# Kernel tuning notes

Measured on AMD Instinct MI355X. Metric: run time of the kernel, lower is better.

Reference implementation:

```python
import jax, jax.numpy as jnp
import numpy as np

N, IN_XC, IN_YC, OUTC, H, W = 8, 512, 256, 256, 96, 96
C2 = OUTC // 2  # 128
K = 3
NUM_LAT = K * K // 2 + 1  # 5


def conv2d(x, w, b=None, pad=0):
    out = jax.lax.conv_general_dilated(
        x, w, window_strides=(1, 1), padding=[(pad, pad), (pad, pad)],
        dimension_numbers=('NCHW', 'OIHW', 'NCHW'))
    if b is not None:
        out = out + b[None, :, None, None]
    return out


def patches3x3(x):
    # torch nn.Unfold(3, padding=1) taps, ordered (kh, kw) row-major -> [N,C,9,H,W]
    n, c, h, w = x.shape
    xp = jnp.pad(x, ((0, 0), (0, 0), (1, 1), (1, 1)))
    cols = [xp[:, :, i:i + h, j:j + w] for i in range(3) for j in range(3)]
    return jnp.stack(cols, axis=2)


def pool_to_3x3(x):
    # AdaptiveAvgPool2d(3) with H,W divisible by 3 == mean over equal bins
    n, c, h, w = x.shape
    return x.reshape(n, c, 3, h // 3, 3, w // 3).mean(axis=(3, 5))


def setup_inputs() -> dict:
    key = jax.random.key(0)
    ks = jax.random.split(key, 24)
    g = lambda i, shape, s=0.05: (jax.random.normal(ks[i], shape, dtype=jnp.float32) * s)
    return {
        'x': jax.random.normal(ks[0], (N, IN_XC, H, W), dtype=jnp.float32),
        'y': jax.random.normal(ks[1], (N, IN_YC, H, W), dtype=jnp.float32),
        # SDFM.down_input: 1x1 conv in_xC -> out_C
        'w_down': g(2, (OUTC, IN_XC, 1, 1)), 'b_down': g(3, (OUTC,)),
        # channel-attention MLP over 3x3 pooled grid
        'w_ce': g(4, (NUM_LAT, K * K)), 'w_gd': g(5, (K * K, NUM_LAT)),
        'bn_g': jnp.ones((C2,), jnp.float32), 'bn_b': jnp.zeros((C2,), jnp.float32),
        # gernerate_kernel_channel: 1x1 conv mid_in_yC -> mid_in_xC (both 128)
        'w_kc': g(6, (C2, C2, 1, 1)), 'b_kc': g(7, (C2,)),
        # gernerate_kernel_spatial: 3x3 conv C2->C2 then 1x1 conv C2->9
        'w_ks1': g(8, (C2, C2, 3, 3)), 'b_ks1': g(9, (C2,)),
        'w_ks2': g(10, (K * K, C2, 1, 1)), 'b_ks2': g(11, (K * K,)),
        # spatial-attention convs (bias=False)
        'w_sp1': g(12, (1, C2, 3, 3)), 'w_sp': g(13, (1, 2, 3, 3)),
        # branch fuse: 3x3 conv out_C -> out_C
        'w_fb': g(14, (OUTC, 2 * C2, 3, 3)), 'b_fb': g(15, (OUTC,)),
        # SDFM.fuse (BasicConv_PRelu): 3x3 conv 2*out_C -> out_C, BN(eval), PReLU
        'w_fuse': g(16, (OUTC, 2 * OUTC, 3, 3)),
        'bn2_g': jnp.ones((OUTC,), jnp.float32), 'bn2_b': jnp.zeros((OUTC,), jnp.float32),
        'prelu_a': jnp.full((OUTC,), 0.25, jnp.float32),
    }


def reference(x, y, w_down, b_down, w_ce, w_gd, bn_g, bn_b, w_kc, b_kc,
              w_ks1, b_ks1, w_ks2, b_ks2, w_sp1, w_sp, w_fb, b_fb,
              w_fuse, bn2_g, bn2_b, prelu_a):
    # SDFM.down_input
    x = conv2d(x, w_down, b_down, pad=0)          # [N, 256, H, W]
    n, c, h, w = x.shape
    c2 = c // 2
    x1, x2 = x[:, :c2], x[:, c2:]                 # [N,128,H,W] each
    y1, y2 = y[:, :c2], y[:, c2:]

    # --- channel branch: per-(sample,channel) dynamic 3x3 depthwise kernel ---
    gl = pool_to_3x3(x1).reshape(n, c2, K * K)    # [N,128,9]
    att = gl @ w_ce.T                              # ce (no bias) -> [N,128,5]
    att = att * bn_g[None, :, None] + bn_b[None, :, None]  # BN1d eval (rm=0, rv=1)
    att = jax.nn.relu(att)
    att = jax.nn.sigmoid(att @ w_gd.T)            # [N,128,9]

    kc = conv2d(pool_to_3x3(y1), w_kc, b_kc, pad=0)  # [N,128,3,3]
    kc = kc.reshape(n, c2, K * K) * att           # [N,128,9]
    # grouped conv (groups = N*C/2) == per-sample depthwise dynamic conv
    channel_after = jnp.einsum('nckhw,nck->nchw', patches3x3(x1), kc)

    # --- spatial branch: per-pixel dynamic 3x3 kernel ---
    ks = conv2d(conv2d(y2, w_ks1, b_ks1, pad=1), w_ks2, b_ks2, pad=0)  # [N,9,H,W]

    ksp = conv2d(x2, w_sp1, None, pad=1)          # [N,1,H,W]
    p = patches3x3(ksp).reshape(n, K * K, h, w)   # [N,9,H,W]
    avg = p.mean(axis=1, keepdims=True)
    mx = p.max(axis=1, keepdims=True)
    sp = jax.nn.sigmoid(conv2d(jnp.concatenate([avg, mx], axis=1), w_sp, None, pad=1))  # [N,1,H,W]

    kernel_after = (ks * sp).transpose(0, 2, 3, 1)[..., None]  # [N,H,W,9,1]

    # faithful replication of the original quirky reshape of unfold output:
    # [N, C2*9, H*W] -> [N, H, W, C2, 9]
    unfold_x = patches3x3(x2).reshape(n, c2 * K * K, h * w).reshape(n, h, w, c2, K * K)
    spatial_after = jnp.matmul(unfold_x, kernel_after)[..., 0]  # [N,H,W,C2]
    spatial_after = spatial_after.transpose(0, 3, 1, 2)          # [N,C2,H,W]

    result = jnp.concatenate([channel_after, spatial_after], axis=1)  # [N,256,H,W]
    r1 = conv2d(result, w_fb, b_fb, pad=1)        # branch fuse 3x3

    # SDFM.fuse: BasicConv_PRelu = conv3x3 (no bias) + BN(eval, rm=0,rv=1) + PReLU
    o = conv2d(jnp.concatenate([x, r1], axis=1), w_fuse, None, pad=1)
    o = o * bn2_g[None, :, None, None] + bn2_b[None, :, None, None]
    o = jnp.where(o >= 0, o, prelu_a[None, :, None, None] * o)
    return o
```

## Files before the change

### kernel.cpp

```cpp
#include <hip/hip_runtime.h>
#include <hip/hip_bf16.h>
#include <math.h>

#define HW 9216
#define IMG 96

typedef __bf16 bf16x8 __attribute__((ext_vector_type(8)));
typedef float  f32x4  __attribute__((ext_vector_type(4)));

__device__ __forceinline__ void gload16(const void* g, void* l) {
    __builtin_amdgcn_global_load_lds((const unsigned int*)g, (unsigned int*)l, 16, 0, 0);
}

#define WAITV(N) asm volatile("s_waitcnt vmcnt(" #N ")" ::: "memory")
#define BARX()   { asm volatile("" ::: "memory"); __builtin_amdgcn_s_barrier(); asm volatile("" ::: "memory"); }

__global__ __launch_bounds__(256) void nchw2nhwc_kernel(
    const float* __restrict__ src, long n_stride_src,
    __hip_bfloat16* __restrict__ dst, int dst_stride)
{
    __shared__ float tile[32][65];
    const int px0 = blockIdx.x * 64;
    const int c0  = blockIdx.y * 32;
    const int n   = blockIdx.z;
    const int tid = threadIdx.x;
    const int tx = tid & 63, ty = tid >> 6;
    #pragma unroll
    for (int i = 0; i < 8; ++i)
        tile[ty + i * 4][tx] = src[n * n_stride_src + (long)(c0 + ty + i * 4) * HW + px0 + tx];
    __syncthreads();
    const int ci = tid & 31, pxl = tid >> 5;
    #pragma unroll
    for (int j = 0; j < 8; ++j) {
        int px = pxl + j * 8;
        dst[((long)n * HW + px0 + px) * dst_stride + c0 + ci] = __float2bfloat16(tile[ci][px]);
    }
}

__global__ __launch_bounds__(256) void wconv_kernel(
    const float* __restrict__ src, __hip_bfloat16* __restrict__ dst,
    int cout, int cin, int taps)
{
    int idx = blockIdx.x * 256 + threadIdx.x;
    if (idx >= cout * cin) return;
    int co = idx / cin, ci = idx % cin;
    for (int t = 0; t < taps; ++t)
        dst[((long)t * cout + co) * cin + ci] = __float2bfloat16(src[(long)idx * taps + t]);
}

template<int CIN, int TAPS, bool SPLIT>
__global__ __launch_bounds__(256, 2) void mfma_conv(
    const __hip_bfloat16* __restrict__ in_a,
    const __hip_bfloat16* __restrict__ in_b,
    const __hip_bfloat16* __restrict__ w_t,
    const float* __restrict__ bias,
    float* __restrict__ out_nchw, long nchw_nstride,
    __hip_bfloat16* __restrict__ out_nhwc, int nhwc_stride,
    int cout,
    const float* __restrict__ bng, const float* __restrict__ bnb,
    const float* __restrict__ pra,
    const __hip_bfloat16* __restrict__ zeropage)
{
    constexpr int ROWS = (TAPS == 9) ? 6 : 4;
    constexpr int COLS = (TAPS == 9) ? 98 : 96;
    constexpr int HOFF = (TAPS == 9) ? 1 : 0;
    constexpr int PSTR = SPLIT ? 256 : CIN;
    constexpr int NSEG_IN = ROWS * COLS * 4;
    constexpr int NSEG_W  = TAPS * 64 * 4;
    constexpr int IN_BYTES = NSEG_IN * 16;
    constexpr int W_BYTES  = NSEG_W * 16;
    constexpr int BUF = IN_BYTES + W_BYTES;
    constexpr int NCHUNK = CIN / 32;
    constexpr int FULL_IN = NSEG_IN / 256;
    constexpr int HAS_TAIL = (NSEG_IN % 256) != 0;
    constexpr int IT_IN = FULL_IN + HAS_TAIL;
    constexpr int IT_W  = NSEG_W / 256;

    extern __shared__ __align__(16) char lds[];

    const int h0   = blockIdx.x * 4;
    const int cob  = blockIdx.y * 64;
    const int n    = blockIdx.z;
    const int tid  = threadIdx.x;
    const int lane = tid & 63;
    const int wave = tid >> 6;
    const int l16  = lane & 15, lg = lane >> 4;

    const long dAB = SPLIT ? ((const char*)in_b - (const char*)in_a - 448) : 0;

    const char* inptr[IT_IN];
    int inval[IT_IN];
    #pragma unroll
    for (int t = 0; t < IT_IN; ++t) {
        int seg = tid + t * 256;
        int s2 = (seg < NSEG_IN) ? seg : 0;
        int pix = s2 >> 2, qp = s2 & 3;
        int r = pix / COLS, c = pix % COLS;
        int h = h0 + r - HOFF, w = c - HOFF;
        int q = qp ^ ((c >> 1) & 3);
        bool valid = (h >= 0 && h < IMG && w >= 0 && w < IMG);
        inptr[t] = valid
            ? (const char*)(in_a + ((long)n * HW + h * IMG + w) * PSTR + q * 8)
            : (const char*)zeropage;
        inval[t] = valid ? 1 : 0;
    }
    const char* wptr[IT_W];
    #pragma unroll
    for (int t = 0; t < IT_W; ++t) {
        int seg = tid + t * 256;
        int tap = seg >> 8, rem = seg & 255;
        int co = rem >> 2, qp = rem & 3;
        int q = qp ^ ((co >> 1) & 3);
        wptr[t] = (const char*)(w_t + ((long)tap * cout + cob + co) * CIN + q * 8);
    }

    auto stage = [&](int bb, long adv) {
        char* ib = lds + bb * BUF;
        char* wb = ib + IN_BYTES;
        #pragma unroll
        for (int t = 0; t < FULL_IN; ++t) {
            int seg = tid + t * 256;
            gload16(inptr[t], ib + seg * 16);
            if (inval[t]) inptr[t] += adv;
        }
        if (HAS_TAIL) {
            int seg = tid + FULL_IN * 256;
            if (seg < NSEG_IN) {
                gload16(inptr[IT_IN - 1], ib + seg * 16);
                if (inval[IT_IN - 1]) inptr[IT_IN - 1] += adv;
            }
        }
        #pragma unroll
        for (int t = 0; t < IT_W; ++t) {
            int seg = tid + t * 256;
            gload16(wptr[t], wb + seg * 16);
            wptr[t] += 64;
        }
    };

    f32x4 acc[4][6];
    #pragma unroll
    for (int m = 0; m < 4; ++m)
        #pragma unroll
        for (int nf = 0; nf < 6; ++nf) acc[m][nf] = (f32x4){0.f, 0.f, 0.f, 0.f};

    const int qa = lg ^ ((l16 >> 1) & 3);
    const int a_off = l16 * 64 + qa * 16;

    stage(0, 64);

    for (int ch = 0; ch < NCHUNK; ++ch) {
        if (ch + 1 < NCHUNK) {
            long adv = (SPLIT && (ch + 1) == 7) ? dAB : 64;
            stage((ch + 1) & 1, adv);
            if constexpr (TAPS == 9) {
                if (wave == 0) { WAITV(19); } else { WAITV(18); }
            } else {
                WAITV(7);
            }
        } else {
            WAITV(0);
        }
        BARX();

        const char* ib = lds + (ch & 1) * BUF;
        const char* wb = ib + IN_BYTES;
        __builtin_amdgcn_s_setprio(1);
        #pragma unroll
        for (int tap = 0; tap < TAPS; ++tap) {
            const int g = (TAPS == 9) ? tap / 3 : 0;
            const int kx = (TAPS == 9) ? tap % 3 : 0;
            bf16x8 a[4];
            #pragma unroll
            for (int m = 0; m < 4; ++m)
                a[m] = *(const bf16x8*)(wb + tap * 4096 + m * 1024 + a_off);
            #pragma unroll
            for (int nf = 0; nf < 6; ++nf) {
                const int c = nf * 16 + l16 + kx;
                const int qb = lg ^ ((c >> 1) & 3);
                bf16x8 b = *(const bf16x8*)(ib + ((wave + g) * COLS + c) * 64 + qb * 16);
                #pragma unroll
                for (int m = 0; m < 4; ++m)
                    acc[m][nf] = __builtin_amdgcn_mfma_f32_16x16x32_bf16(a[m], b, acc[m][nf], 0, 0, 0);
            }
        }
        __builtin_amdgcn_s_setprio(0);
        BARX();
    }

    const int hrow = h0 + wave;
    #pragma unroll
    for (int m = 0; m < 4; ++m) {
        const int co = cob + m * 16 + lg * 4;
        float bs[4], g4[4], b4[4], p4[4];
        #pragma unroll
        for (int r = 0; r < 4; ++r) bs[r] = bias ? bias[co + r] : 0.f;
        if (bng) {
            #pragma unroll
            for (int r = 0; r < 4; ++r) { g4[r] = bng[co + r]; b4[r] = bnb[co + r]; p4[r] = pra[co + r]; }
        }
        #pragma unroll
        for (int nf = 0; nf < 6; ++nf) {
            const int wcol = nf * 16 + l16;
            const long px = (long)hrow * IMG + wcol;
            float v[4];
            #pragma unroll
            for (int r = 0; r < 4; ++r) {
                v[r] = acc[m][nf][r] + bs[r];
                if (bng) {
                    v[r] = v[r] * g4[r] + b4[r];
                    v[r] = (v[r] >= 0.f) ? v[r] : p4[r] * v[r];
                }
            }
            if (out_nchw) {
                #pragma unroll
                for (int r = 0; r < 4; ++r)
                    out_nchw[(long)n * nchw_nstride + (long)(co + r) * HW + px] = v[r];
            }
            if (out_nhwc) {
                union { __hip_bfloat16 h[4]; uint2 u; } pk;
                #pragma unroll
                for (int r = 0; r < 4; ++r) pk.h[r] = __float2bfloat16(v[r]);
                *reinterpret_cast<uint2*>(&out_nhwc[((long)n * HW + px) * nhwc_stride + co]) = pk.u;
            }
        }
    }
}

__global__ __launch_bounds__(256) void pool_kernel(
    const float* __restrict__ xd, const float* __restrict__ y,
    float* __restrict__ gl, float* __restrict__ py)
{
    const int c = blockIdx.x, n = blockIdx.y, which = blockIdx.z;
    const int tid = threadIdx.x;
    const float* src = (which == 0) ? (xd + ((long)n * 256 + c) * HW)
                                    : (y  + ((long)n * 256 + c) * HW);
    float local[9];
    #pragma unroll
    for (int k = 0; k < 9; ++k) local[k] = 0.f;
    for (int i = tid; i < HW; i += 256) {
        int h = i / 96, w = i % 96;
        local[(h / 32) * 3 + (w / 32)] += src[i];
    }
    __shared__ float red[9][4];
    const int wv = tid >> 6, lane = tid & 63;
    #pragma unroll
    for (int k = 0; k < 9; ++k) {
        float v = local[k];
        for (int off = 32; off > 0; off >>= 1) v += __shfl_down(v, off, 64);
        if (lane == 0) red[k][wv] = v;
    }
    __syncthreads();
    if (tid < 9) {
        float s = (red[tid][0] + red[tid][1] + red[tid][2] + red[tid][3]) * (1.f / 1024.f);
        float* dst = (which == 0) ? gl : py;
        dst[((long)n * 128 + c) * 9 + tid] = s;
    }
}

__global__ __launch_bounds__(128) void attkc_kernel(
    const float* __restrict__ gl, const float* __restrict__ py,
    const float* __restrict__ w_ce, const float* __restrict__ w_gd,
    const float* __restrict__ bng, const float* __restrict__ bnb,
    const float* __restrict__ w_kc, const float* __restrict__ b_kc,
    float* __restrict__ kc)
{
    const int n = blockIdx.x, c = threadIdx.x;
    __shared__ float py_s[128][9];
    #pragma unroll
    for (int k = 0; k < 9; ++k) py_s[c][k] = py[((long)n * 128 + c) * 9 + k];
    __syncthreads();
    float g[9];
    #pragma unroll
    for (int k = 0; k < 9; ++k) g[k] = gl[((long)n * 128 + c) * 9 + k];
    float t[5];
    #pragma unroll
    for (int l = 0; l < 5; ++l) {
        float s = 0.f;
        #pragma unroll
        for (int k = 0; k < 9; ++k) s += g[k] * w_ce[l * 9 + k];
        s = s * bng[c] + bnb[c];
        t[l] = s > 0.f ? s : 0.f;
    }
    float att[9];
    #pragma unroll
    for (int k = 0; k < 9; ++k) {
        float s = 0.f;
        #pragma unroll
        for (int l = 0; l < 5; ++l) s += t[l] * w_gd[k * 5 + l];
        att[k] = 1.f / (1.f + expf(-s));
    }
    float kc0[9];
    float bk = b_kc[c];
    #pragma unroll
    for (int k = 0; k < 9; ++k) kc0[k] = bk;
    for (int c2 = 0; c2 < 128; ++c2) {
        float wv = w_kc[c * 128 + c2];
        #pragma unroll
        for (int k = 0; k < 9; ++k) kc0[k] += wv * py_s[c2][k];
    }
    #pragma unroll
    for (int k = 0; k < 9; ++k)
        kc[((long)n * 128 + c) * 9 + k] = kc0[k] * att[k];
}

__global__ __launch_bounds__(256) void channel_nhwc_kernel(
    const __hip_bfloat16* __restrict__ catx, const float* __restrict__ kc,
    __hip_bfloat16* __restrict__ catfb)
{
    const int h  = blockIdx.x;
    const int n  = blockIdx.y;
    const int cg = (threadIdx.x & 15) * 8;
    const int w0 = threadIdx.x >> 4;
    float k9[8][9];
    #pragma unroll
    for (int j = 0; j < 8; ++j)
        #pragma unroll
        for (int t = 0; t < 9; ++t) k9[j][t] = kc[((long)n * 128 + cg + j) * 9 + t];
    const long pbase = (long)n * HW;
    for (int it = 0; it < 6; ++it) {
        const int w = w0 + it * 16;
        float acc[8];
        #pragma unroll
        for (int j = 0; j < 8; ++j) acc[j] = 0.f;
        #pragma unroll
        for (int ky = 0; ky < 3; ++ky) {
            const int hh = h + ky - 1;
            if (hh < 0 || hh >= IMG) continue;
            #pragma unroll
            for (int kx = 0; kx < 3; ++kx) {
                const int ww = w + kx - 1;
                if (ww < 0 || ww >= IMG) continue;
                bf16x8 v = *reinterpret_cast<const bf16x8*>(
                    &catx[(pbase + hh * IMG + ww) * 256 + cg]);
                #pragma unroll
                for (int j = 0; j < 8; ++j)
                    acc[j] += k9[j][ky * 3 + kx] * (float)v[j];
            }
        }
        union { __hip_bfloat16 hh[8]; uint4 u; } pk;
        #pragma unroll
        for (int j = 0; j < 8; ++j) pk.hh[j] = __float2bfloat16(acc[j]);
        *reinterpret_cast<uint4*>(&catfb[(pbase + h * IMG + w) * 256 + cg]) = pk.u;
    }
}

__global__ __launch_bounds__(256) void ks_kernel(
    const float* __restrict__ ksmid, const float* __restrict__ w_ks2,
    const float* __restrict__ b_ks2, float* __restrict__ ks)
{
    __shared__ float w_s[9 * 128];
    const int tid = threadIdx.x;
    for (int i = tid; i < 1152; i += 256) w_s[i] = w_ks2[i];
    __syncthreads();
    const int p = blockIdx.x * 256 + tid;
    const int n = blockIdx.y;
    float acc[9];
    #pragma unroll
    for (int k = 0; k < 9; ++k) acc[k] = b_ks2[k];
    for (int c = 0; c < 128; ++c) {
        float v = ksmid[((long)n * 128 + c) * HW + p];
        #pragma unroll
        for (int k = 0; k < 9; ++k) acc[k] += w_s[k * 128 + c] * v;
    }
    #pragma unroll
    for (int k = 0; k < 9; ++k) ks[((long)n * 9 + k) * HW + p] = acc[k];
}

__global__ __launch_bounds__(256) void ksp_nhwc_kernel(
    const __hip_bfloat16* __restrict__ catx, const float* __restrict__ w_sp1,
    float* __restrict__ ksp)
{
    __shared__ float w_s[9][128];
    const int tid = threadIdx.x;
    for (int i = tid; i < 1152; i += 256) {
        int ci = i / 9, tap = i % 9;
        w_s[tap][ci] = w_sp1[i];
    }
    __syncthreads();
    const int p = blockIdx.x * 256 + tid;
    const int n = blockIdx.y;
    const int h = p / 96, w = p % 96;
    const long pbase = (long)n * HW;
    float acc = 0.f;
    #pragma unroll
    for (int ky = 0; ky < 3; ++ky) {
        const int hh = h + ky - 1;
        if (hh < 0 || hh >= IMG) continue;
        #pragma unroll
        for (int kx = 0; kx < 3; ++kx) {
            const int ww = w + kx - 1;
            if (ww < 0 || ww >= IMG) continue;
            const int tap = ky * 3 + kx;
            const __hip_bfloat16* row = &catx[(pbase + hh * IMG + ww) * 256 + 128];
            #pragma unroll
            for (int vq = 0; vq < 16; ++vq) {
                bf16x8 v = *reinterpret_cast<const bf16x8*>(&row[vq * 8]);
                #pragma unroll
                for (int j = 0; j < 8; ++j)
                    acc += w_s[tap][vq * 8 + j] * (float)v[j];
            }
        }
    }
    ksp[pbase + p] = acc;
}

__global__ __launch_bounds__(256) void sp_kernel(
    const float* __restrict__ ksp, const float* __restrict__ w_sp,
    float* __restrict__ sp)
{
    const int p = blockIdx.x * 256 + threadIdx.x;
    const int n = blockIdx.y;
    const int h = p / 96, w = p % 96;
    const float* kp = ksp + (long)n * HW;
    float acc = 0.f;
    #pragma unroll
    for (int dy = 0; dy < 3; ++dy)
        #pragma unroll
        for (int dx = 0; dx < 3; ++dx) {
            int hh = h + dy - 1, ww = w + dx - 1;
            if (hh < 0 || hh >= 96 || ww < 0 || ww >= 96) continue;
            float s = 0.f, m = -1e30f;
            #pragma unroll
            for (int iy = 0; iy < 3; ++iy)
                #pragma unroll
                for (int ix = 0; ix < 3; ++ix) {
                    int h2 = hh + iy - 1, w2 = ww + ix - 1;
                    float v = (h2 >= 0 && h2 < 96 && w2 >= 0 && w2 < 96) ? kp[h2 * 96 + w2] : 0.f;
                    s += v; m = fmaxf(m, v);
                }
            acc += w_sp[dy * 3 + dx] * (s * (1.f / 9.f)) + w_sp[9 + dy * 3 + dx] * m;
        }
    sp[(long)n * HW + p] = 1.f / (1.f + expf(-acc));
}

__global__ __launch_bounds__(256) void spatial_kernel(
    const float* __restrict__ xd, const float* __restrict__ ks,
    const float* __restrict__ sp, __hip_bfloat16* __restrict__ catfb)
{
    const int cc = blockIdx.x;
    const int n  = blockIdx.y;
    const int tid = threadIdx.x;
    __shared__ float plane[HW];
    const float* src = xd + ((long)n * 256 + 128 + cc) * HW;
    for (int i = tid; i < HW / 4; i += 256)
        *reinterpret_cast<float4*>(&plane[i * 4]) = *reinterpret_cast<const float4*>(&src[i * 4]);
    __syncthreads();
    const int c  = tid & 127;
    const int pr = tid >> 7;
    const int c9 = c * 9;
    for (int j = 0; j < 36; ++j) {
        const int pl = pr + j * 2;
        const int p  = cc * 72 + pl;
        float spv = sp[(long)n * HW + p];
        float kv[9];
        #pragma unroll
        for (int k = 0; k < 9; ++k) kv[k] = ks[((long)n * 9 + k) * HW + p] * spv;
        const int base = pl * 1152 + c9;
        int kk0 = base / 9216;
        int r20 = base - kk0 * 9216;
        int h20 = r20 / 96;
        int w20 = r20 - h20 * 96;
        float acc = 0.f;
        #pragma unroll
        for (int k = 0; k < 9; ++k) {
            int kk = kk0, h2 = h20, w2 = w20 + k;
            if (w2 >= 96) { h2 += 1; w2 -= 96; }
            if (h2 >= 96) { kk += 1; h2 -= 96; }
            int hh = h2 + kk / 3 - 1;
            int ww = w2 + kk % 3 - 1;
            float v = (hh >= 0 && hh < 96 && ww >= 0 && ww < 96) ? plane[hh * 96 + ww] : 0.f;
            acc += v * kv[k];
        }
        catfb[((long)n * HW + p) * 256 + 128 + c] = __float2bfloat16(acc);
    }
}

extern "C" void kernel_launch(void* const* d_in, const int* in_sizes, int n_in,
                              void* d_out, int out_size, void* d_ws, size_t ws_size,
                              hipStream_t stream)
{
    const float* x      = (const float*)d_in[0];
    const float* y      = (const float*)d_in[1];
    const float* w_down = (const float*)d_in[2];
    const float* b_down = (const float*)d_in[3];
    const float* w_ce   = (const float*)d_in[4];
    const float* w_gd   = (const float*)d_in[5];
    const float* bn_g   = (const float*)d_in[6];
    const float* bn_b   = (const float*)d_in[7];
    const float* w_kc   = (const float*)d_in[8];
    const float* b_kc   = (const float*)d_in[9];
    const float* w_ks1  = (const float*)d_in[10];
    const float* b_ks1  = (const float*)d_in[11];
    const float* w_ks2  = (const float*)d_in[12];
    const float* b_ks2  = (const float*)d_in[13];
    const float* w_sp1  = (const float*)d_in[14];
    const float* w_sp   = (const float*)d_in[15];
    const float* w_fb   = (const float*)d_in[16];
    const float* b_fb   = (const float*)d_in[17];
    const float* w_fuse = (const float*)d_in[18];
    const float* bn2_g  = (const float*)d_in[19];
    const float* bn2_b  = (const float*)d_in[20];
    const float* prelu  = (const float*)d_in[21];
    float* out = (float*)d_out;
    char* ws = (char*)d_ws;

    const long HWl = HW;
    float* xd = (float*)ws;                               ws += 8L * 256 * HWl * 4;
    char* region2 = ws;                                   ws += 8L * HWl * 512 * 2;
    __hip_bfloat16* x_t    = (__hip_bfloat16*)region2;
    __hip_bfloat16* cat_r1 = (__hip_bfloat16*)region2;
    float*          ksmid  = (float*)region2;
    __hip_bfloat16* catfb  = (__hip_bfloat16*)(region2 + 8L * HWl * 256 * 2);
    __hip_bfloat16* cat_x  = (__hip_bfloat16*)ws;         ws += 8L * HWl * 256 * 2;
    __hip_bfloat16* y2t    = (__hip_bfloat16*)ws;         ws += 8L * HWl * 128 * 2;
    __hip_bfloat16* wdown_bf = (__hip_bfloat16*)ws;       ws += 1L * 256 * 512 * 2;
    __hip_bfloat16* wks1_bf  = (__hip_bfloat16*)ws;       ws += 9L * 128 * 128 * 2;
    __hip_bfloat16* wfb_bf   = (__hip_bfloat16*)ws;       ws += 9L * 256 * 256 * 2;
    __hip_bfloat16* wfuse_bf = (__hip_bfloat16*)ws;       ws += 9L * 256 * 512 * 2;
    float* ks   = (float*)ws;  ws += 8L * 9 * HWl * 4;
    float* ksp  = (float*)ws;  ws += 8L * HWl * 4;
    float* spb  = (float*)ws;  ws += 8L * HWl * 4;
    float* gl   = (float*)ws;  ws += 8L * 128 * 9 * 4;
    float* py   = (float*)ws;  ws += 8L * 128 * 9 * 4;
    float* kc   = (float*)ws;  ws += 8L * 128 * 9 * 4;
    __hip_bfloat16* zp = (__hip_bfloat16*)ws;  ws += 256;

    hipMemsetAsync((void*)zp, 0, 256, stream);

    wconv_kernel<<<dim3(512), 256, 0, stream>>>(w_down, wdown_bf, 256, 512, 1);
    wconv_kernel<<<dim3(64),  256, 0, stream>>>(w_ks1,  wks1_bf,  128, 128, 9);
    wconv_kernel<<<dim3(256), 256, 0, stream>>>(w_fb,   wfb_bf,   256, 256, 9);
    wconv_kernel<<<dim3(512), 256, 0, stream>>>(w_fuse, wfuse_bf, 256, 512, 9);

    nchw2nhwc_kernel<<<dim3(144, 16, 8), 256, 0, stream>>>(x, 512L * HWl, x_t, 512);
    mfma_conv<512, 1, false><<<dim3(24, 4, 8), 256, 57344, stream>>>(
        x_t, nullptr, wdown_bf, b_down, xd, 256L * HWl, cat_x, 256, 256,
        nullptr, nullptr, nullptr, zp);

    nchw2nhwc_kernel<<<dim3(144, 4, 8), 256, 0, stream>>>(y + 128L * HWl, 256L * HWl, y2t, 128);

    pool_kernel<<<dim3(128, 8, 2), 256, 0, stream>>>(xd, y, gl, py);
    attkc_kernel<<<dim3(8), 128, 0, stream>>>(gl, py, w_ce, w_gd, bn_g, bn_b, w_kc, b_kc, kc);

    mfma_conv<128, 9, false><<<dim3(24, 2, 8), 256, 148992, stream>>>(
        y2t, nullptr, wks1_bf, b_ks1, ksmid, 128L * HWl, nullptr, 0, 128,
        nullptr, nullptr, nullptr, zp);
    ks_kernel<<<dim3(36, 8), 256, 0, stream>>>(ksmid, w_ks2, b_ks2, ks);

    ksp_nhwc_kernel<<<dim3(36, 8), 256, 0, stream>>>(cat_x, w_sp1, ksp);
    sp_kernel<<<dim3(36, 8), 256, 0, stream>>>(ksp, w_sp, spb);

    spatial_kernel<<<dim3(128, 8), 256, 0, stream>>>(xd, ks, spb, catfb);
    channel_nhwc_kernel<<<dim3(96, 8), 256, 0, stream>>>(cat_x, kc, catfb);

    mfma_conv<256, 9, false><<<dim3(24, 4, 8), 256, 148992, stream>>>(
        catfb, nullptr, wfb_bf, b_fb, nullptr, 0, cat_r1, 256, 256,
        nullptr, nullptr, nullptr, zp);

    mfma_conv<512, 9, true><<<dim3(24, 4, 8), 256, 148992, stream>>>(
        cat_x, cat_r1, wfuse_bf, nullptr, out, 256L * HWl, nullptr, 0, 256,
        bn2_g, bn2_b, prelu, zp);
}
```

Baseline: 678.1 us.

## Load conv weights directly into registers and software-pipeline by tap group

```diff
diff --git a/kernel.cpp b/kernel.cpp
--- a/kernel.cpp
+++ b/kernel.cpp
@@ -12,8 +12,9 @@
     __builtin_amdgcn_global_load_lds((const unsigned int*)g, (unsigned int*)l, 16, 0, 0);
 }
 
-#define WAITV(N) asm volatile("s_waitcnt vmcnt(" #N ")" ::: "memory")
+#define WAITV0() asm volatile("s_waitcnt vmcnt(0)" ::: "memory")
 #define BARX()   { asm volatile("" ::: "memory"); __builtin_amdgcn_s_barrier(); asm volatile("" ::: "memory"); }
+#define SB0()    __builtin_amdgcn_sched_barrier(0)
 
 __global__ __launch_bounds__(256) void nchw2nhwc_kernel(
     const float* __restrict__ src, long n_stride_src,
@@ -66,15 +67,13 @@
     constexpr int HOFF = (TAPS == 9) ? 1 : 0;
     constexpr int PSTR = SPLIT ? 256 : CIN;
     constexpr int NSEG_IN = ROWS * COLS * 4;
-    constexpr int NSEG_W  = TAPS * 64 * 4;
     constexpr int IN_BYTES = NSEG_IN * 16;
-    constexpr int W_BYTES  = NSEG_W * 16;
-    constexpr int BUF = IN_BYTES + W_BYTES;
     constexpr int NCHUNK = CIN / 32;
     constexpr int FULL_IN = NSEG_IN / 256;
     constexpr int HAS_TAIL = (NSEG_IN % 256) != 0;
     constexpr int IT_IN = FULL_IN + HAS_TAIL;
-    constexpr int IT_W  = NSEG_W / 256;
+    constexpr int TPG = (TAPS == 9) ? 3 : 1;
+    constexpr int NW = TPG * 4;
 
     extern __shared__ __align__(16) char lds[];
 
@@ -104,19 +103,9 @@
             : (const char*)zeropage;
         inval[t] = valid ? 1 : 0;
     }
-    const char* wptr[IT_W];
-    #pragma unroll
-    for (int t = 0; t < IT_W; ++t) {
-        int seg = tid + t * 256;
-        int tap = seg >> 8, rem = seg & 255;
-        int co = rem >> 2, qp = rem & 3;
-        int q = qp ^ ((co >> 1) & 3);
-        wptr[t] = (const char*)(w_t + ((long)tap * cout + cob + co) * CIN + q * 8);
-    }
 
     auto stage = [&](int bb, long adv) {
-        char* ib = lds + bb * BUF;
-        char* wb = ib + IN_BYTES;
+        char* ib = lds + bb * IN_BYTES;
         #pragma unroll
         for (int t = 0; t < FULL_IN; ++t) {
             int seg = tid + t * 256;
@@ -130,63 +119,85 @@
                 if (inval[IT_IN - 1]) inptr[IT_IN - 1] += adv;
             }
         }
-        #pragma unroll
-        for (int t = 0; t < IT_W; ++t) {
-            int seg = tid + t * 256;
-            gload16(wptr[t], wb + seg * 16);
-            wptr[t] += 64;
-        }
     };
 
+    const __hip_bfloat16* wlane = w_t + (long)(cob + l16) * CIN + lg * 8;
+
     f32x4 acc[4][6];
     #pragma unroll
     for (int m = 0; m < 4; ++m)
         #pragma unroll
         for (int nf = 0; nf < 6; ++nf) acc[m][nf] = (f32x4){0.f, 0.f, 0.f, 0.f};
 
-    const int qa = lg ^ ((l16 >> 1) & 3);
-    const int a_off = l16 * 64 + qa * 16;
+    bf16x8 wA[NW], wB[NW];
+
+#define LOADW(WREG, CI0, G)                                                   \
+    _Pragma("unroll")                                                         \
+    for (int t3 = 0; t3 < TPG; ++t3)                                          \
+        _Pragma("unroll")                                                     \
+        for (int m = 0; m < 4; ++m)                                           \
+            WREG[t3 * 4 + m] = *(const bf16x8*)(wlane +                       \
+                ((long)(((G) * TPG + t3) * cout + m * 16)) * CIN + (CI0));
+
+#define MFMAG(WREG, IB, G)                                                    \
+    __builtin_amdgcn_s_setprio(1);                                            \
+    _Pragma("unroll")                                                         \
+    for (int t3 = 0; t3 < TPG; ++t3) {                                        \
+        _Pragma("unroll")                                                     \
+        for (int nf = 0; nf < 6; ++nf) {                                      \
+            const int c = nf * 16 + l16 + ((TAPS == 9) ? t3 : 0);             \
+            const int qb = lg ^ ((c >> 1) & 3);                               \
+            bf16x8 b = *(const bf16x8*)((IB) +                                \
+                (((wave + (G)) * COLS) + c) * 64 + qb * 16);                  \
+            _Pragma("unroll")                                                 \
+            for (int m = 0; m < 4; ++m)                                       \
+                acc[m][nf] = __builtin_amdgcn_mfma_f32_16x16x32_bf16(         \
+                    WREG[t3 * 4 + m], b, acc[m][nf], 0, 0, 0);                \
+        }                                                                     \
+    }                                                                         \
+    __builtin_amdgcn_s_setprio(0);
 
     stage(0, 64);
-
-    for (int ch = 0; ch < NCHUNK; ++ch) {
-        if (ch + 1 < NCHUNK) {
-            long adv = (SPLIT && (ch + 1) == 7) ? dAB : 64;
-            stage((ch + 1) & 1, adv);
-            if constexpr (TAPS == 9) {
-                if (wave == 0) { WAITV(19); } else { WAITV(18); }
-            } else {
-                WAITV(7);
-            }
+    LOADW(wA, 0, 0);
+    WAITV0(); BARX();
+
+    const char* ib0 = lds;
+    const char* ib1 = lds + IN_BYTES;
+
+    for (int pc = 0; pc < NCHUNK; pc += 2) {
+        const int c0 = pc * 32, c1 = c0 + 32, c2 = c0 + 64;
+        const long adv1 = (SPLIT && (pc + 1) == 7) ? dAB : 64;
+        const long adv2 = (SPLIT && (pc + 2) == 7) ? dAB : 64;
+
+        if constexpr (TAPS == 9) {
+            LOADW(wB, c0, 1);
+            stage(1, adv1);
+            SB0(); MFMAG(wA, ib0, 0);
+            LOADW(wA, c0, 2);
+            SB0(); MFMAG(wB, ib0, 1);
+            LOADW(wB, c1, 0);
+            SB0(); MFMAG(wA, ib0, 2);
+            WAITV0(); BARX();
+            LOADW(wA, c1, 1);
+            if (pc + 2 < NCHUNK) stage(0, adv2);
+            SB0(); MFMAG(wB, ib1, 0);
+            LOADW(wB, c1, 2);
+            SB0(); MFMAG(wA, ib1, 1);
+            if (pc + 2 < NCHUNK) { LOADW(wA, c2, 0); }
+            SB0(); MFMAG(wB, ib1, 2);
+            WAITV0(); BARX();
         } else {
-            WAITV(0);
-        }
-        BARX();
-
-        const char* ib = lds + (ch & 1) * BUF;
-        const char* wb = ib + IN_BYTES;
-        __builtin_amdgcn_s_setprio(1);
-        #pragma unroll
-        for (int tap = 0; tap < TAPS; ++tap) {
-            const int g = (TAPS == 9) ? tap / 3 : 0;
-            const int kx = (TAPS == 9) ? tap % 3 : 0;
-            bf16x8 a[4];
-            #pragma unroll
-            for (int m = 0; m < 4; ++m)
-                a[m] = *(const bf16x8*)(wb + tap * 4096 + m * 1024 + a_off);
-            #pragma unroll
-            for (int nf = 0; nf < 6; ++nf) {
-                const int c = nf * 16 + l16 + kx;
-                const int qb = lg ^ ((c >> 1) & 3);
-                bf16x8 b = *(const bf16x8*)(ib + ((wave + g) * COLS + c) * 64 + qb * 16);
-                #pragma unroll
-                for (int m = 0; m < 4; ++m)
-                    acc[m][nf] = __builtin_amdgcn_mfma_f32_16x16x32_bf16(a[m], b, acc[m][nf], 0, 0, 0);
-            }
-        }
-        __builtin_amdgcn_s_setprio(0);
-        BARX();
-    }
+            LOADW(wB, c1, 0);
+            stage(1, adv1);
+            SB0(); MFMAG(wA, ib0, 0);
+            WAITV0(); BARX();
+            if (pc + 2 < NCHUNK) { LOADW(wA, c2, 0); stage(0, adv2); }
+            SB0(); MFMAG(wB, ib1, 0);
+            WAITV0(); BARX();
+        }
+    }
+#undef LOADW
+#undef MFMAG
 
     const int hrow = h0 + wave;
     #pragma unroll
@@ -534,7 +545,7 @@
     wconv_kernel<<<dim3(512), 256, 0, stream>>>(w_fuse, wfuse_bf, 256, 512, 9);
 
     nchw2nhwc_kernel<<<dim3(144, 16, 8), 256, 0, stream>>>(x, 512L * HWl, x_t, 512);
-    mfma_conv<512, 1, false><<<dim3(24, 4, 8), 256, 57344, stream>>>(
+    mfma_conv<512, 1, false><<<dim3(24, 4, 8), 256, 49152, stream>>>(
         x_t, nullptr, wdown_bf, b_down, xd, 256L * HWl, cat_x, 256, 256,
         nullptr, nullptr, nullptr, zp);
 
@@ -543,7 +554,7 @@
     pool_kernel<<<dim3(128, 8, 2), 256, 0, stream>>>(xd, y, gl, py);
     attkc_kernel<<<dim3(8), 128, 0, stream>>>(gl, py, w_ce, w_gd, bn_g, bn_b, w_kc, b_kc, kc);
 
-    mfma_conv<128, 9, false><<<dim3(24, 2, 8), 256, 148992, stream>>>(
+    mfma_conv<128, 9, false><<<dim3(24, 2, 8), 256, 75264, stream>>>(
         y2t, nullptr, wks1_bf, b_ks1, ksmid, 128L * HWl, nullptr, 0, 128,
         nullptr, nullptr, nullptr, zp);
     ks_kernel<<<dim3(36, 8), 256, 0, stream>>>(ksmid, w_ks2, b_ks2, ks);
@@ -554,11 +565,11 @@
     spatial_kernel<<<dim3(128, 8), 256, 0, stream>>>(xd, ks, spb, catfb);
     channel_nhwc_kernel<<<dim3(96, 8), 256, 0, stream>>>(cat_x, kc, catfb);
 
-    mfma_conv<256, 9, false><<<dim3(24, 4, 8), 256, 148992, stream>>>(
+    mfma_conv<256, 9, false><<<dim3(24, 4, 8), 256, 75264, stream>>>(
         catfb, nullptr, wfb_bf, b_fb, nullptr, 0, cat_r1, 256, 256,
         nullptr, nullptr, nullptr, zp);
 
-    mfma_conv<512, 9, true><<<dim3(24, 4, 8), 256, 148992, stream>>>(
+    mfma_conv<512, 9, true><<<dim3(24, 4, 8), 256, 75264, stream>>>(
         cat_x, cat_r1, wfuse_bf, nullptr, out, 256L * HWl, nullptr, 0, 256,
         bn2_g, bn2_b, prelu, zp);
 }
```

Result: slower. 1.737 ms (+156.2%).

## Retile MFMA conv to 512-thread blocks covering 8 rows by 32 output channels

Applied to the files above, without the earlier changes.

```diff
diff --git a/kernel.cpp b/kernel.cpp
--- a/kernel.cpp
+++ b/kernel.cpp
@@ -12,8 +12,8 @@
     __builtin_amdgcn_global_load_lds((const unsigned int*)g, (unsigned int*)l, 16, 0, 0);
 }
 
-#define WAITV(N) asm volatile("s_waitcnt vmcnt(" #N ")" ::: "memory")
-#define BARX()   { asm volatile("" ::: "memory"); __builtin_amdgcn_s_barrier(); asm volatile("" ::: "memory"); }
+#define WAITVN(N) asm volatile("s_waitcnt vmcnt(" #N ")" ::: "memory")
+#define BARX()    { asm volatile("" ::: "memory"); __builtin_amdgcn_s_barrier(); asm volatile("" ::: "memory"); }
 
 __global__ __launch_bounds__(256) void nchw2nhwc_kernel(
     const float* __restrict__ src, long n_stride_src,
@@ -49,7 +49,7 @@
 }
 
 template<int CIN, int TAPS, bool SPLIT>
-__global__ __launch_bounds__(256, 2) void mfma_conv(
+__global__ __launch_bounds__(512, 1) void mfma_conv(
     const __hip_bfloat16* __restrict__ in_a,
     const __hip_bfloat16* __restrict__ in_b,
     const __hip_bfloat16* __restrict__ w_t,
@@ -61,25 +61,26 @@
     const float* __restrict__ pra,
     const __hip_bfloat16* __restrict__ zeropage)
 {
-    constexpr int ROWS = (TAPS == 9) ? 6 : 4;
+    constexpr int ROWS = (TAPS == 9) ? 10 : 8;
     constexpr int COLS = (TAPS == 9) ? 98 : 96;
     constexpr int HOFF = (TAPS == 9) ? 1 : 0;
     constexpr int PSTR = SPLIT ? 256 : CIN;
     constexpr int NSEG_IN = ROWS * COLS * 4;
-    constexpr int NSEG_W  = TAPS * 64 * 4;
+    constexpr int NSEG_W  = TAPS * 32 * 4;
     constexpr int IN_BYTES = NSEG_IN * 16;
-    constexpr int W_BYTES  = NSEG_W * 16;
-    constexpr int BUF = IN_BYTES + W_BYTES;
+    constexpr int BUF = IN_BYTES + NSEG_W * 16;
     constexpr int NCHUNK = CIN / 32;
-    constexpr int FULL_IN = NSEG_IN / 256;
-    constexpr int HAS_TAIL = (NSEG_IN % 256) != 0;
-    constexpr int IT_IN = FULL_IN + HAS_TAIL;
-    constexpr int IT_W  = NSEG_W / 256;
+    constexpr int FULL_IN = NSEG_IN / 512;
+    constexpr int IN_TAIL = NSEG_IN % 512;
+    constexpr int FULL_W  = NSEG_W / 512;
+    constexpr int W_TAIL  = NSEG_W % 512;
+    constexpr int IT_IN = FULL_IN + (IN_TAIL ? 1 : 0);
+    constexpr int IT_W  = FULL_W + (W_TAIL ? 1 : 0);
 
     extern __shared__ __align__(16) char lds[];
 
-    const int h0   = blockIdx.x * 4;
-    const int cob  = blockIdx.y * 64;
+    const int h0   = blockIdx.x * 8;
+    const int cob  = blockIdx.y * 32;
     const int n    = blockIdx.z;
     const int tid  = threadIdx.x;
     const int lane = tid & 63;
@@ -92,7 +93,7 @@
     int inval[IT_IN];
     #pragma unroll
     for (int t = 0; t < IT_IN; ++t) {
-        int seg = tid + t * 256;
+        int seg = tid + t * 512;
         int s2 = (seg < NSEG_IN) ? seg : 0;
         int pix = s2 >> 2, qp = s2 & 3;
         int r = pix / COLS, c = pix % COLS;
@@ -107,8 +108,9 @@
     const char* wptr[IT_W];
     #pragma unroll
     for (int t = 0; t < IT_W; ++t) {
-        int seg = tid + t * 256;
-        int tap = seg >> 8, rem = seg & 255;
+        int seg = tid + t * 512;
+        int s2 = (seg < NSEG_W) ? seg : 0;
+        int tap = s2 >> 7, rem = s2 & 127;
         int co = rem >> 2, qp = rem & 3;
         int q = qp ^ ((co >> 1) & 3);
         wptr[t] = (const char*)(w_t + ((long)tap * cout + cob + co) * CIN + q * 8);
@@ -119,28 +121,31 @@
         char* wb = ib + IN_BYTES;
         #pragma unroll
         for (int t = 0; t < FULL_IN; ++t) {
-            int seg = tid + t * 256;
-            gload16(inptr[t], ib + seg * 16);
+            gload16(inptr[t], ib + (tid + t * 512) * 16);
             if (inval[t]) inptr[t] += adv;
         }
-        if (HAS_TAIL) {
-            int seg = tid + FULL_IN * 256;
-            if (seg < NSEG_IN) {
-                gload16(inptr[IT_IN - 1], ib + seg * 16);
+        if (IN_TAIL) {
+            if (tid < IN_TAIL) {
+                gload16(inptr[IT_IN - 1], ib + (tid + FULL_IN * 512) * 16);
                 if (inval[IT_IN - 1]) inptr[IT_IN - 1] += adv;
             }
         }
         #pragma unroll
-        for (int t = 0; t < IT_W; ++t) {
-            int seg = tid + t * 256;
-            gload16(wptr[t], wb + seg * 16);
+        for (int t = 0; t < FULL_W; ++t) {
+            gload16(wptr[t], wb + (tid + t * 512) * 16);
             wptr[t] += 64;
         }
+        if (W_TAIL) {
+            if (tid < W_TAIL) {
+                gload16(wptr[IT_W - 1], wb + (tid + FULL_W * 512) * 16);
+                wptr[IT_W - 1] += 64;
+            }
+        }
     };
 
-    f32x4 acc[4][6];
-    #pragma unroll
-    for (int m = 0; m < 4; ++m)
+    f32x4 acc[2][6];
+    #pragma unroll
+    for (int m = 0; m < 2; ++m)
         #pragma unroll
         for (int nf = 0; nf < 6; ++nf) acc[m][nf] = (f32x4){0.f, 0.f, 0.f, 0.f};
 
@@ -148,18 +153,19 @@
     const int a_off = l16 * 64 + qa * 16;
 
     stage(0, 64);
+    WAITVN(0); BARX();
 
     for (int ch = 0; ch < NCHUNK; ++ch) {
         if (ch + 1 < NCHUNK) {
             long adv = (SPLIT && (ch + 1) == 7) ? dAB : 64;
             stage((ch + 1) & 1, adv);
             if constexpr (TAPS == 9) {
-                if (wave == 0) { WAITV(19); } else { WAITV(18); }
+                if (wave < 2) { WAITVN(11); } else if (wave < 6) { WAITVN(10); } else { WAITVN(9); }
             } else {
-                WAITV(7);
+                if (wave < 2) { WAITVN(7); } else { WAITVN(6); }
             }
         } else {
-            WAITV(0);
+            WAITVN(0);
         }
         BARX();
 
@@ -170,18 +176,15 @@
         for (int tap = 0; tap < TAPS; ++tap) {
             const int g = (TAPS == 9) ? tap / 3 : 0;
             const int kx = (TAPS == 9) ? tap % 3 : 0;
-            bf16x8 a[4];
-            #pragma unroll
-            for (int m = 0; m < 4; ++m)
-                a[m] = *(const bf16x8*)(wb + tap * 4096 + m * 1024 + a_off);
+            bf16x8 a0 = *(const bf16x8*)(wb + tap * 2048 + a_off);
+            bf16x8 a1 = *(const bf16x8*)(wb + tap * 2048 + 1024 + a_off);
             #pragma unroll
             for (int nf = 0; nf < 6; ++nf) {
                 const int c = nf * 16 + l16 + kx;
                 const int qb = lg ^ ((c >> 1) & 3);
                 bf16x8 b = *(const bf16x8*)(ib + ((wave + g) * COLS + c) * 64 + qb * 16);
-                #pragma unroll
-                for (int m = 0; m < 4; ++m)
-                    acc[m][nf] = __builtin_amdgcn_mfma_f32_16x16x32_bf16(a[m], b, acc[m][nf], 0, 0, 0);
+                acc[0][nf] = __builtin_amdgcn_mfma_f32_16x16x32_bf16(a0, b, acc[0][nf], 0, 0, 0);
+                acc[1][nf] = __builtin_amdgcn_mfma_f32_16x16x32_bf16(a1, b, acc[1][nf], 0, 0, 0);
             }
         }
         __builtin_amdgcn_s_setprio(0);
@@ -190,7 +193,7 @@
 
     const int hrow = h0 + wave;
     #pragma unroll
-    for (int m = 0; m < 4; ++m) {
+    for (int m = 0; m < 2; ++m) {
         const int co = cob + m * 16 + lg * 4;
         float bs[4], g4[4], b4[4], p4[4];
         #pragma unroll
@@ -526,7 +529,7 @@
     float* kc   = (float*)ws;  ws += 8L * 128 * 9 * 4;
     __hip_bfloat16* zp = (__hip_bfloat16*)ws;  ws += 256;
 
-    hipMemsetAsync((void*)zp, 0, 256, stream);
+    (void)hipMemsetAsync((void*)zp, 0, 256, stream);
 
     wconv_kernel<<<dim3(512), 256, 0, stream>>>(w_down, wdown_bf, 256, 512, 1);
     wconv_kernel<<<dim3(64),  256, 0, stream>>>(w_ks1,  wks1_bf,  128, 128, 9);
@@ -534,7 +537,7 @@
     wconv_kernel<<<dim3(512), 256, 0, stream>>>(w_fuse, wfuse_bf, 256, 512, 9);
 
     nchw2nhwc_kernel<<<dim3(144, 16, 8), 256, 0, stream>>>(x, 512L * HWl, x_t, 512);
-    mfma_conv<512, 1, false><<<dim3(24, 4, 8), 256, 57344, stream>>>(
+    mfma_conv<512, 1, false><<<dim3(12, 8, 8), 512, 102400, stream>>>(
         x_t, nullptr, wdown_bf, b_down, xd, 256L * HWl, cat_x, 256, 256,
         nullptr, nullptr, nullptr, zp);
 
@@ -543,7 +546,7 @@
     pool_kernel<<<dim3(128, 8, 2), 256, 0, stream>>>(xd, y, gl, py);
     attkc_kernel<<<dim3(8), 128, 0, stream>>>(gl, py, w_ce, w_gd, bn_g, bn_b, w_kc, b_kc, kc);
 
-    mfma_conv<128, 9, false><<<dim3(24, 2, 8), 256, 148992, stream>>>(
+    mfma_conv<128, 9, false><<<dim3(12, 4, 8), 512, 162304, stream>>>(
         y2t, nullptr, wks1_bf, b_ks1, ksmid, 128L * HWl, nullptr, 0, 128,
         nullptr, nullptr, nullptr, zp);
     ks_kernel<<<dim3(36, 8), 256, 0, stream>>>(ksmid, w_ks2, b_ks2, ks);
@@ -554,11 +557,11 @@
     spatial_kernel<<<dim3(128, 8), 256, 0, stream>>>(xd, ks, spb, catfb);
     channel_nhwc_kernel<<<dim3(96, 8), 256, 0, stream>>>(cat_x, kc, catfb);
 
-    mfma_conv<256, 9, false><<<dim3(24, 4, 8), 256, 148992, stream>>>(
+    mfma_conv<256, 9, false><<<dim3(12, 8, 8), 512, 162304, stream>>>(
         catfb, nullptr, wfb_bf, b_fb, nullptr, 0, cat_r1, 256, 256,
         nullptr, nullptr, nullptr, zp);
 
-    mfma_conv<512, 9, true><<<dim3(24, 4, 8), 256, 148992, stream>>>(
+    mfma_conv<512, 9, true><<<dim3(12, 8, 8), 512, 162304, stream>>>(
         cat_x, cat_r1, wfuse_bf, nullptr, out, 256L * HWl, nullptr, 0, 256,
         bn2_g, bn2_b, prelu, zp);
 }
```

After: 671.6 us. No clear change (-1.0%).
